# Kernel tuning notes

Hardware: AMD Instinct MI355X
Metric: run time of the kernel (lower is better)

Reference implementation:

```python
import jax, jax.numpy as jnp
import numpy as np

N = 100000        # nodes (== node_num)
E = 3200000       # edges
C = 8             # hidden (sparse=False branch)
HEADS = 2
GROUPS = 8
LAYERS = 3
FEAT = 16
EMB = 8
NCLS = 2


def glin(x, W, b):
    # PyG grouped Linear: x [..., C], W [G, C//G, C//G], b [C]
    G, cin, cout = W.shape
    xg = x.reshape(*x.shape[:-1], G, cin)
    out = jnp.einsum('...gi,gio->...go', xg, W)
    return out.reshape(*x.shape[:-1], G * cout) + b


def gcn_norm(edge_index, num_nodes):
    # symmetric GCN normalization with added self-loops, unit edge weights
    loop = jnp.arange(num_nodes, dtype=edge_index.dtype)
    src = jnp.concatenate([edge_index[0], loop])
    dst = jnp.concatenate([edge_index[1], loop])
    w = jnp.ones(src.shape[0], dtype=jnp.float32)
    deg = jax.ops.segment_sum(w, dst, num_segments=num_nodes)
    dinv = jnp.where(deg > 0, jax.lax.rsqrt(deg), 0.0)
    return src, dst, dinv[src] * dinv[dst]


def dna_conv(x_all, src, dst, norm, Wq, bq, Wk, bk, Wv, bv):
    # PyG DNAConv (eval mode): target's latest history entry attends over the
    # source neighbor's full history. x_all: [N, L, C].
    n, L, c = x_all.shape
    d = c // HEADS
    # q/k/v linears are per-entry -> compute per node, gather per edge (same math)
    q = glin(x_all[:, -1], Wq, bq).reshape(n, HEADS, d)    # [N,H,d]
    k = glin(x_all, Wk, bk).reshape(n, L, HEADS, d)        # [N,L,H,d]
    v = glin(x_all, Wv, bv).reshape(n, L, HEADS, d)
    qe = q[dst]                                            # [E',H,d]
    score = jnp.einsum('ehd,elhd->ehl', qe, k[src]) * (1.0 / np.sqrt(d))
    attn = jax.nn.softmax(score, axis=-1)                  # softmax over history L
    out = jnp.einsum('ehl,elhd->ehd', attn, v[src]).reshape(-1, c)
    out = out * norm[:, None]
    return jax.ops.segment_sum(out, dst, num_segments=n)   # aggr='add' at target


def setup_inputs():
    ks = jax.random.split(jax.random.key(0), 16)
    s = 0.5
    return {
        'x': jax.random.normal(ks[0], (N, FEAT), dtype=jnp.float32),
        'node_index': jnp.arange(N),
        'node_one_hot': jnp.zeros((N,), dtype=jnp.int32),
        'edge_index': jax.random.randint(ks[1], (2, E), 0, N),
        'edge_weight': jax.random.uniform(ks[2], (E,), dtype=jnp.float32),
        'emb_table': jax.random.normal(ks[3], (N, EMB), dtype=jnp.float32) * 0.1,
        'W1': jax.random.normal(ks[4], (EMB + FEAT, C), dtype=jnp.float32) * 0.2,
        'b1': jnp.zeros((C,), dtype=jnp.float32),
        'Wq': jax.random.normal(ks[5], (LAYERS, GROUPS, C // GROUPS, C // GROUPS), dtype=jnp.float32) * s,
        'bq': jnp.zeros((LAYERS, C), dtype=jnp.float32),
        'Wk': jax.random.normal(ks[6], (LAYERS, GROUPS, C // GROUPS, C // GROUPS), dtype=jnp.float32) * s,
        'bk': jnp.zeros((LAYERS, C), dtype=jnp.float32),
        'Wv': jax.random.normal(ks[7], (LAYERS, GROUPS, C // GROUPS, C // GROUPS), dtype=jnp.float32) * s,
        'bv': jnp.zeros((LAYERS, C), dtype=jnp.float32),
        'W2': jax.random.normal(ks[8], (C, NCLS), dtype=jnp.float32) * 0.3,
        'b2': jnp.zeros((NCLS,), dtype=jnp.float32),
    }


def reference(x, node_index, node_one_hot, edge_index, edge_weight,
              emb_table, W1, b1, Wq, bq, Wk, bk, Wv, bv, W2, b2):
    # node_one_hot / edge_weight are unpacked but unused in the original forward
    h = jnp.concatenate([emb_table[node_index], x], axis=1)   # [N, EMB+FEAT]
    h = jax.nn.relu(h @ W1 + b1)                              # [N, C]
    x_all = h[:, None, :]                                     # history [N, 1, C]
    src, dst, norm = gcn_norm(edge_index, x.shape[0])
    for i in range(LAYERS):
        h = jax.nn.relu(dna_conv(x_all, src, dst, norm,
                                 Wq[i], bq[i], Wk[i], bk[i], Wv[i], bv[i]))
        x_all = jnp.concatenate([x_all, h[:, None, :]], axis=1)
    logits = x_all[:, -1] @ W2 + b2
    return jax.nn.log_softmax(logits, axis=-1)
```

## Files before the change

### kernel.cpp

```cpp
#include <hip/hip_runtime.h>
#include <math.h>


#define SBB   8
#define SBN   256
#define CH    4096
#define CAP   9216

typedef _Float16 half8 __attribute__((ext_vector_type(8)));
typedef int int4v __attribute__((ext_vector_type(4)));

__global__ void __launch_bounds__(256) phaseAC(const int* __restrict__ eidx,
                                               int* __restrict__ gcnt,
                                               int* __restrict__ ebuf,
                                               int E, int NS) {
    __shared__ int sorted_[CH];
    __shared__ unsigned short karr[CH];
    __shared__ int cntS[512];
    __shared__ int lofs[512];
    __shared__ int wbase[512];
    __shared__ int sA[512], sB[512];
    int t = threadIdx.x, b = blockIdx.x;
    int base = b * CH;
    int nEdge = E - base; if (nEdge > CH) nEdge = CH;

    for (int i = t; i < 512; i += 256) cntS[i] = 0;
    __syncthreads();

    int w[16]; short kk[16];
#pragma unroll
    for (int it = 0; it < 4; it++) {
        int e0 = base + (it * 256 + t) * 4;
        if (e0 + 3 < E) {
            int4v s4 = __builtin_nontemporal_load((const int4v*)(eidx + e0));
            int4v d4 = __builtin_nontemporal_load((const int4v*)(eidx + E + e0));
#pragma unroll
            for (int j = 0; j < 4; j++) {
                int idx = it * 4 + j;
                w[idx] = s4[j] | ((d4[j] & (SBN - 1)) << 17);
                kk[idx] = (short)(d4[j] >> SBB);
                atomicAdd(&cntS[kk[idx]], 1);
            }
        } else {
#pragma unroll
            for (int j = 0; j < 4; j++) {
                int e = e0 + j, idx = it * 4 + j;
                if (e < E) {
                    int s = eidx[e], d = eidx[E + e];
                    w[idx] = s | ((d & (SBN - 1)) << 17);
                    kk[idx] = (short)(d >> SBB);
                    atomicAdd(&cntS[kk[idx]], 1);
                } else { w[idx] = 0; kk[idx] = 511; }
            }
        }
    }
    __syncthreads();
    sA[t] = cntS[t]; sA[t + 256] = cntS[t + 256];
    __syncthreads();
    int* sp = sA; int* dp = sB;
    for (int o = 1; o < 512; o <<= 1) {
#pragma unroll
        for (int h = 0; h < 2; h++) {
            int i = t + h * 256;
            int v = sp[i];
            if (i >= o) v += sp[i - o];
            dp[i] = v;
        }
        __syncthreads();
        int* tmp = sp; sp = dp; dp = tmp;
    }
    for (int i = t; i < 512; i += 256) {
        int excl = sp[i] - cntS[i];
        lofs[i] = excl;
        if (i < NS && cntS[i] > 0) {
            int g = atomicAdd(&gcnt[i], cntS[i]);
            wbase[i] = i * CAP + g - excl;
        }
    }
    __syncthreads();
#pragma unroll
    for (int idx = 0; idx < 16; idx++) {
        if (kk[idx] != 511) {
            int p = atomicAdd(&lofs[kk[idx]], 1);
            sorted_[p] = w[idx];
            karr[p] = (unsigned short)kk[idx];
        }
    }
    __syncthreads();
    for (int i = t; i < nEdge; i += 256)
        ebuf[wbase[karr[i]] + i] = sorted_[i];
}

__global__ void super_csr(int* __restrict__ ebuf, const int* __restrict__ gcnt,
                          unsigned int* __restrict__ off, char* __restrict__ A,
                          char* __restrict__ U, int NS, int n) {
    __shared__ int seg[CAP];
    __shared__ int cnt[SBN];
    __shared__ int fillp[SBN];
    __shared__ int sd[256];
    int t = threadIdx.x, k = blockIdx.x;
    cnt[t] = 0;
    int start = k * CAP;
    int len = gcnt[k];
    __syncthreads();
    for (int i = t; i < len; i += 256) {
        int w = __builtin_nontemporal_load(&ebuf[start + i]);
        seg[i] = w;
        atomicAdd(&cnt[w >> 17], 1);
    }
    __syncthreads();
    int v = cnt[t];
    sd[t] = v; __syncthreads();
    for (int o = 1; o < 256; o <<= 1) {
        int u = 0; if (t >= o) u = sd[t - o];
        __syncthreads(); sd[t] += u; __syncthreads();
    }
    int excl = sd[t] - v;
    fillp[t] = excl;
    int d = (k << SBB) + t;
    if (d < n) {
        off[d] = (unsigned int)(start + excl) | ((unsigned int)v << 22);
        float dvv = rsqrtf((float)(v + 1));
        *(float*)(A + (size_t)d * 32 + 16) = dvv;
        *(float*)(U + (size_t)d * 64 + 48) = dvv;
    }
    __syncthreads();
    for (int i = t; i < len; i += 256) {
        int w = seg[i];
        int pos = atomicAdd(&fillp[w >> 17], 1);
        ebuf[start + pos] = w & 131071;
    }
}

__global__ void node_init(const float* __restrict__ x, const int* __restrict__ nidx,
                          const float* __restrict__ emb, const float* __restrict__ W1,
                          const float* __restrict__ b1, char* __restrict__ A,
                          char* __restrict__ U, int* __restrict__ gcnt,
                          int NS, int n) {
    int i = blockIdx.x * blockDim.x + threadIdx.x;
    if (i < NS) gcnt[i] = 0;
    if (i >= n) return;
    float in[24];
    int ni = nidx[i];
    const float4* ep = (const float4*)(emb + (size_t)ni * 8);
    float4 e0 = ep[0], e1 = ep[1];
    in[0] = e0.x; in[1] = e0.y; in[2] = e0.z; in[3] = e0.w;
    in[4] = e1.x; in[5] = e1.y; in[6] = e1.z; in[7] = e1.w;
    const float4* xp = (const float4*)(x + (size_t)i * 16);
#pragma unroll
    for (int t = 0; t < 4; t++) {
        float4 v = xp[t];
        in[8 + 4 * t + 0] = v.x; in[8 + 4 * t + 1] = v.y;
        in[8 + 4 * t + 2] = v.z; in[8 + 4 * t + 3] = v.w;
    }
    float acc[8];
#pragma unroll
    for (int j = 0; j < 8; j++) acc[j] = b1[j];
#pragma unroll
    for (int t = 0; t < 24; t++) {
        float xv = in[t];
#pragma unroll
        for (int j = 0; j < 8; j++) acc[j] = fmaf(xv, W1[t * 8 + j], acc[j]);
    }
    half8 h;
#pragma unroll
    for (int j = 0; j < 8; j++) h[j] = (_Float16)fmaxf(acc[j], 0.0f);
    *(half8*)(A + (size_t)i * 32) = h;
    *(half8*)(U + (size_t)i * 64) = h;
}

template <int Li, bool LAST>
__global__ void __launch_bounds__(256)
agg_layer(int* __restrict__ ssrc, const unsigned int* __restrict__ off,
          const char* __restrict__ A, char* __restrict__ U,
          const float* __restrict__ wq, const float* __restrict__ bq,
          const float* __restrict__ wk, const float* __restrict__ bk,
          const float* __restrict__ wv, const float* __restrict__ bv,
          const float* __restrict__ W2, const float* __restrict__ b2,
          float* __restrict__ out, int n) {
    constexpr int B = (Li == 1) ? 8 : 4;
    constexpr int STEP = 8 * B;
    int tid = blockIdx.x * blockDim.x + threadIdx.x;
    int d = tid >> 3, t = tid & 7;
    if (d >= n) return;
    unsigned int ow = off[d];
    int lo = (int)(ow & 0x3FFFFFu), cnt = (int)(ow >> 22);
    int* sp = ssrc + lo - 1;

    float nd, SN;
    if (Li == 1) {
        nd = *(const float*)(A + (size_t)d * 32 + 16);
        SN = 0.f;
    } else {
        float2 nn = *(const float2*)(U + (size_t)d * 64 + 48);
        nd = nn.x; SN = nn.y;
    }

    float qk[8];
    if (Li >= 2) {
        half8 qh = (Li == 2) ? *(const half8*)(U + (size_t)d * 64 + 16)
                             : *(const half8*)(U + (size_t)d * 64 + 32);
#pragma unroll
        for (int c = 0; c < 8; c++) {
            float qv = fmaf((float)qh[c], wq[c], bq[c]);
            qk[c] = 0.72134752f * wk[c] * qv;
        }
    }

    float T[8];
#pragma unroll
    for (int c = 0; c < 8; c++) T[c] = 0.f;

    int total = cnt + 1;

    int s0 = t;
    unsigned int wcur[B];
    int mcur = 0;
    if (s0 < total) {
        mcur = (total - s0 + 7) >> 3; if (mcur > B) mcur = B;
#pragma unroll
        for (int u = 0; u < B; u++) {
            int s = s0 + 8 * u;
            wcur[u] = 0u;
            if (u < mcur && s > 0) wcur[u] = (unsigned int)sp[s];
        }
    }

    while (s0 < total) {
        int m = mcur;
        int si[B]; float ns[B];
        half8 r[B][Li];
#pragma unroll
        for (int u = 0; u < B; u++) {
            if (u < m) {
                int s = s0 + 8 * u;
                si[u] = (s == 0) ? d : (int)(wcur[u] & 0x1FFFFu);
                if (Li == 1) {
                    const char* p = A + (size_t)si[u] * 32;
                    r[u][0] = *(const half8*)p;
                    ns[u] = (s == 0) ? nd : *(const float*)(p + 16);
                } else {
                    const char* p = U + (size_t)si[u] * 64;
#pragma unroll
                    for (int l = 0; l < Li; l++) r[u][l] = *(const half8*)(p + l * 16);
                    ns[u] = (s == 0) ? nd : (float)(wcur[u] >> 17) * (1.0f / 32767.0f);
                }
            }
        }
        int s1 = s0 + STEP;
        unsigned int wnext[B];
        int mnext = 0;
        if (s1 < total) {
            mnext = (total - s1 + 7) >> 3; if (mnext > B) mnext = B;
#pragma unroll
            for (int u = 0; u < B; u++) {
                wnext[u] = 0u;
                if (u < mnext) wnext[u] = (unsigned int)sp[s1 + 8 * u];
            }
        }
#pragma unroll
        for (int u = 0; u < B; u++) {
            if (u < m) {
                float xs[8 * Li];
#pragma unroll
                for (int l = 0; l < Li; l++)
#pragma unroll
                    for (int c = 0; c < 8; c++) xs[l * 8 + c] = (float)r[u][l][c];
                float nv = ns[u];
                if (Li == 1) {
#pragma unroll
                    for (int c = 0; c < 8; c++) T[c] = fmaf(nv, xs[c], T[c]);
                    SN += nv;
                } else {
                    float score[2][Li];
#pragma unroll
                    for (int l = 0; l < Li; l++) {
#pragma unroll
                        for (int h = 0; h < 2; h++) {
                            float sc = 0.f;
#pragma unroll
                            for (int dd = 0; dd < 4; dd++) {
                                int c = h * 4 + dd;
                                sc = fmaf(qk[c], xs[l * 8 + c], sc);
                            }
                            score[h][l] = sc;
                        }
                    }
                    float f[2][Li];
                    if (Li == 2) {
#pragma unroll
                        for (int h = 0; h < 2; h++) {
                            float g = exp2f(score[h][1] - score[h][0]);
                            float inv = nv * __builtin_amdgcn_rcpf(1.0f + g);
                            f[h][0] = inv; f[h][1] = inv * g;
                        }
                    } else {
#pragma unroll
                        for (int h = 0; h < 2; h++) {
                            float ssum = 0.f;
#pragma unroll
                            for (int l = 0; l < Li; l++) { f[h][l] = exp2f(score[h][l]); ssum += f[h][l]; }
                            float nsh = nv * __builtin_amdgcn_rcpf(ssum);
#pragma unroll
                            for (int l = 0; l < Li; l++) f[h][l] *= nsh;
                        }
                    }
#pragma unroll
                    for (int c = 0; c < 8; c++) {
                        int h = c >> 2;
#pragma unroll
                        for (int l = 0; l < Li; l++) T[c] = fmaf(f[h][l], xs[l * 8 + c], T[c]);
                    }
                }
            }
        }
        if (Li == 1) {
#pragma unroll
            for (int u = 0; u < B; u++) {
                int s = s0 + 8 * u;
                if (u < m && s > 0) {
                    unsigned int q = (unsigned int)(ns[u] * 32767.0f + 0.5f);
                    sp[s] = (int)(wcur[u] | (q << 17));
                }
            }
        }
        s0 = s1; mcur = mnext;
#pragma unroll
        for (int u = 0; u < B; u++) wcur[u] = wnext[u];
    }
#pragma unroll
    for (int m2 = 1; m2 < 8; m2 <<= 1) {
#pragma unroll
        for (int c = 0; c < 8; c++) T[c] += __shfl_xor(T[c], m2);
        if (Li == 1) SN += __shfl_xor(SN, m2);
    }
    if (!LAST) {
        float acc = fmaf(wv[t], T[t], bv[t] * SN);
        float h = fmaxf(acc * nd, 0.f);
        *(_Float16*)(U + (size_t)d * 64 + Li * 16 + 2 * t) = (_Float16)h;
        if (Li == 1 && t == 1)
            *(float*)(U + (size_t)d * 64 + 52) = SN;
    } else if (t == 0) {
        float z0 = b2[0], z1 = b2[1];
#pragma unroll
        for (int c = 0; c < 8; c++) {
            float acc = fmaf(wv[c], T[c], bv[c] * SN);
            float h = fmaxf(acc * nd, 0.f);
            z0 = fmaf(h, W2[c * 2 + 0], z0);
            z1 = fmaf(h, W2[c * 2 + 1], z1);
        }
        float m2 = fmaxf(z0, z1);
        float lse = m2 + logf(__expf(z0 - m2) + __expf(z1 - m2));
        ((float2*)out)[d] = make_float2(z0 - lse, z1 - lse);
    }
}

extern "C" void kernel_launch(void* const* d_in, const int* in_sizes, int n_in,
                              void* d_out, int out_size, void* d_ws, size_t ws_size,
                              hipStream_t stream) {
    const float* x    = (const float*)d_in[0];
    const int*   nidx = (const int*)d_in[1];
    const int*   eidx = (const int*)d_in[3];
    const float* emb  = (const float*)d_in[5];
    const float* W1   = (const float*)d_in[6];
    const float* b1   = (const float*)d_in[7];
    const float* Wq   = (const float*)d_in[8];
    const float* bq   = (const float*)d_in[9];
    const float* Wk   = (const float*)d_in[10];
    const float* bk   = (const float*)d_in[11];
    const float* Wv   = (const float*)d_in[12];
    const float* bv   = (const float*)d_in[13];
    const float* W2   = (const float*)d_in[14];
    const float* b2   = (const float*)d_in[15];
    float* out = (float*)d_out;

    const int n = in_sizes[0] / 16;
    const int E = in_sizes[3] / 2;
    const int NS = (n + SBN - 1) / SBN;
    const int NBLK = (E + CH - 1) / CH;

    char* wsp = (char*)d_ws;
    char*  A     = wsp;                      wsp += (size_t)n * 32;
    char*  U     = wsp;                      wsp += (size_t)n * 64;
    int*   ebuf  = (int*)wsp;                wsp += (size_t)NS * CAP * 4;
    unsigned int* off = (unsigned int*)wsp;  wsp += (size_t)n * 4;
    int*   gcnt  = (int*)wsp;                wsp += (size_t)NS * 4;

    dim3 blk(256);
    dim3 gn((n + 255) / 256);
    dim3 ga(((size_t)n * 8 + 255) / 256);

    node_init<<<gn, blk, 0, stream>>>(x, nidx, emb, W1, b1, A, U, gcnt, NS, n);
    phaseAC<<<NBLK, blk, 0, stream>>>(eidx, gcnt, ebuf, E, NS);
    super_csr<<<NS, blk, 0, stream>>>(ebuf, gcnt, off, A, U, NS, n);

    agg_layer<1, false><<<ga, blk, 0, stream>>>(ebuf, off, A, U,
        Wq, bq, Wk, bk, Wv, bv, W2, b2, out, n);
    agg_layer<2, false><<<ga, blk, 0, stream>>>(ebuf, off, A, U,
        Wq + 8, bq + 8, Wk + 8, bk + 8, Wv + 8, bv + 8, W2, b2, out, n);
    agg_layer<3, true><<<ga, blk, 0, stream>>>(ebuf, off, A, U,
        Wq + 16, bq + 16, Wk + 16, bk + 16, Wv + 16, bv + 16, W2, b2, out, n);
}
```

Baseline: 274.8 us.

## Split interleaved node history records into separate per-layer feature arrays

Replaces the packed per-node records (a 32-byte A record and a 64-byte U record holding the history, norms and SN) with separate 16-byte fp16 arrays per layer (H0, H1, H2) plus standalone norm arrays NRM and ND. Gathers in each aggregation layer now touch one to three separate 16-byte rows instead of one contiguous 32- or 64-byte row. The aim is to cut wasted bytes in the first layers and the duplicated write of h0. The cost is that layers 2 and 3 issue more scattered cache-line accesses per gathered neighbor, and layer 1 does an extra gather for the source norm.

```diff
diff --git a/kernel.cpp b/kernel.cpp
--- a/kernel.cpp
+++ b/kernel.cpp
@@ -92,8 +92,8 @@
 }
 
 __global__ void super_csr(int* __restrict__ ebuf, const int* __restrict__ gcnt,
-                          unsigned int* __restrict__ off, char* __restrict__ A,
-                          char* __restrict__ U, int NS, int n) {
+                          unsigned int* __restrict__ off, float* __restrict__ NRM,
+                          float* __restrict__ ND, int NS, int n) {
     __shared__ int seg[CAP];
     __shared__ int cnt[SBN];
     __shared__ int fillp[SBN];
@@ -121,8 +121,8 @@
     if (d < n) {
         off[d] = (unsigned int)(start + excl) | ((unsigned int)v << 22);
         float dvv = rsqrtf((float)(v + 1));
-        *(float*)(A + (size_t)d * 32 + 16) = dvv;
-        *(float*)(U + (size_t)d * 64 + 48) = dvv;
+        NRM[d] = dvv;
+        ND[2 * (size_t)d] = dvv;
     }
     __syncthreads();
     for (int i = t; i < len; i += 256) {
@@ -134,9 +134,8 @@
 
 __global__ void node_init(const float* __restrict__ x, const int* __restrict__ nidx,
                           const float* __restrict__ emb, const float* __restrict__ W1,
-                          const float* __restrict__ b1, char* __restrict__ A,
-                          char* __restrict__ U, int* __restrict__ gcnt,
-                          int NS, int n) {
+                          const float* __restrict__ b1, char* __restrict__ H0,
+                          int* __restrict__ gcnt, int NS, int n) {
     int i = blockIdx.x * blockDim.x + threadIdx.x;
     if (i < NS) gcnt[i] = 0;
     if (i >= n) return;
@@ -165,14 +164,15 @@
     half8 h;
 #pragma unroll
     for (int j = 0; j < 8; j++) h[j] = (_Float16)fmaxf(acc[j], 0.0f);
-    *(half8*)(A + (size_t)i * 32) = h;
-    *(half8*)(U + (size_t)i * 64) = h;
+    *(half8*)(H0 + (size_t)i * 16) = h;
 }
 
 template <int Li, bool LAST>
 __global__ void __launch_bounds__(256)
 agg_layer(int* __restrict__ ssrc, const unsigned int* __restrict__ off,
-          const char* __restrict__ A, char* __restrict__ U,
+          const char* __restrict__ H0, char* __restrict__ H1,
+          char* __restrict__ H2, const float* __restrict__ NRM,
+          float* __restrict__ ND,
           const float* __restrict__ wq, const float* __restrict__ bq,
           const float* __restrict__ wk, const float* __restrict__ bk,
           const float* __restrict__ wv, const float* __restrict__ bv,
@@ -189,17 +189,17 @@
 
     float nd, SN;
     if (Li == 1) {
-        nd = *(const float*)(A + (size_t)d * 32 + 16);
+        nd = NRM[d];
         SN = 0.f;
     } else {
-        float2 nn = *(const float2*)(U + (size_t)d * 64 + 48);
+        float2 nn = *(const float2*)(ND + 2 * (size_t)d);
         nd = nn.x; SN = nn.y;
     }
 
     float qk[8];
     if (Li >= 2) {
-        half8 qh = (Li == 2) ? *(const half8*)(U + (size_t)d * 64 + 16)
-                             : *(const half8*)(U + (size_t)d * 64 + 32);
+        half8 qh = (Li == 2) ? *(const half8*)(H1 + (size_t)d * 16)
+                             : *(const half8*)(H2 + (size_t)d * 16);
 #pragma unroll
         for (int c = 0; c < 8; c++) {
             float qv = fmaf((float)qh[c], wq[c], bq[c]);
@@ -235,14 +235,12 @@
             if (u < m) {
                 int s = s0 + 8 * u;
                 si[u] = (s == 0) ? d : (int)(wcur[u] & 0x1FFFFu);
+                r[u][0] = *(const half8*)(H0 + (size_t)si[u] * 16);
+                if (Li >= 2) r[u][1] = *(const half8*)(H1 + (size_t)si[u] * 16);
+                if (Li >= 3) r[u][2] = *(const half8*)(H2 + (size_t)si[u] * 16);
                 if (Li == 1) {
-                    const char* p = A + (size_t)si[u] * 32;
-                    r[u][0] = *(const half8*)p;
-                    ns[u] = (s == 0) ? nd : *(const float*)(p + 16);
+                    ns[u] = (s == 0) ? nd : NRM[si[u]];
                 } else {
-                    const char* p = U + (size_t)si[u] * 64;
-#pragma unroll
-                    for (int l = 0; l < Li; l++) r[u][l] = *(const half8*)(p + l * 16);
                     ns[u] = (s == 0) ? nd : (float)(wcur[u] >> 17) * (1.0f / 32767.0f);
                 }
             }
@@ -337,9 +335,10 @@
     if (!LAST) {
         float acc = fmaf(wv[t], T[t], bv[t] * SN);
         float h = fmaxf(acc * nd, 0.f);
-        *(_Float16*)(U + (size_t)d * 64 + Li * 16 + 2 * t) = (_Float16)h;
+        char* Hout = (Li == 1) ? H1 : H2;
+        *(_Float16*)(Hout + (size_t)d * 16 + 2 * t) = (_Float16)h;
         if (Li == 1 && t == 1)
-            *(float*)(U + (size_t)d * 64 + 52) = SN;
+            ND[2 * (size_t)d + 1] = SN;
     } else if (t == 0) {
         float z0 = b2[0], z1 = b2[1];
 #pragma unroll
@@ -380,8 +379,11 @@
     const int NBLK = (E + CH - 1) / CH;
 
     char* wsp = (char*)d_ws;
-    char*  A     = wsp;                      wsp += (size_t)n * 32;
-    char*  U     = wsp;                      wsp += (size_t)n * 64;
+    char*  H0    = wsp;                      wsp += (size_t)n * 16;
+    char*  H1    = wsp;                      wsp += (size_t)n * 16;
+    char*  H2    = wsp;                      wsp += (size_t)n * 16;
+    float* ND    = (float*)wsp;              wsp += (size_t)n * 8;
+    float* NRM   = (float*)wsp;              wsp += (size_t)n * 4;
     int*   ebuf  = (int*)wsp;                wsp += (size_t)NS * CAP * 4;
     unsigned int* off = (unsigned int*)wsp;  wsp += (size_t)n * 4;
     int*   gcnt  = (int*)wsp;                wsp += (size_t)NS * 4;
@@ -390,14 +392,14 @@
     dim3 gn((n + 255) / 256);
     dim3 ga(((size_t)n * 8 + 255) / 256);
 
-    node_init<<<gn, blk, 0, stream>>>(x, nidx, emb, W1, b1, A, U, gcnt, NS, n);
+    node_init<<<gn, blk, 0, stream>>>(x, nidx, emb, W1, b1, H0, gcnt, NS, n);
     phaseAC<<<NBLK, blk, 0, stream>>>(eidx, gcnt, ebuf, E, NS);
-    super_csr<<<NS, blk, 0, stream>>>(ebuf, gcnt, off, A, U, NS, n);
-
-    agg_layer<1, false><<<ga, blk, 0, stream>>>(ebuf, off, A, U,
+    super_csr<<<NS, blk, 0, stream>>>(ebuf, gcnt, off, NRM, ND, NS, n);
+
+    agg_layer<1, false><<<ga, blk, 0, stream>>>(ebuf, off, H0, H1, H2, NRM, ND,
         Wq, bq, Wk, bk, Wv, bv, W2, b2, out, n);
-    agg_layer<2, false><<<ga, blk, 0, stream>>>(ebuf, off, A, U,
+    agg_layer<2, false><<<ga, blk, 0, stream>>>(ebuf, off, H0, H1, H2, NRM, ND,
         Wq + 8, bq + 8, Wk + 8, bk + 8, Wv + 8, bv + 8, W2, b2, out, n);
-    agg_layer<3, true><<<ga, blk, 0, stream>>>(ebuf, off, A, U,
+    agg_layer<3, true><<<ga, blk, 0, stream>>>(ebuf, off, H0, H1, H2, NRM, ND,
         Wq + 16, bq + 16, Wk + 16, bk + 16, Wv + 16, bv + 16, W2, b2, out, n);
 }
```

New measurement: 291.7 us. 1.06x slower.
